# Kernel optimization log

Hardware: AMD Instinct MI355X
Metric: run time of the kernel (lower is better)

The kernel has to match this reference:

```python
import jax, jax.numpy as jnp
import numpy as np

N, E, D, H, G, L = 50000, 800000, 64, 2, 512, 3  # nodes, edges, hidden, heads, graphs, layers


def setup_inputs() -> dict:
    key = jax.random.key(0)
    ks = jax.random.split(key, 20)
    x = jax.random.normal(ks[0], (N, D), dtype=jnp.float32)
    edge_index = jax.random.randint(ks[1], (2, E), 0, N, dtype=jnp.int64)
    batch = jnp.sort(jax.random.randint(ks[2], (N,), 0, G, dtype=jnp.int64))
    s = 1.0 / np.sqrt(D)
    Wq = jax.random.normal(ks[3], (L, D, H * D), dtype=jnp.float32) * s
    bq = jnp.zeros((L, H * D), jnp.float32)
    Wk = jax.random.normal(ks[4], (L, D, H * D), dtype=jnp.float32) * s
    bk = jnp.zeros((L, H * D), jnp.float32)
    Wv = jax.random.normal(ks[5], (L, D, H * D), dtype=jnp.float32) * s
    bv = jnp.zeros((L, H * D), jnp.float32)
    Ws = jax.random.normal(ks[6], (L, D, D), dtype=jnp.float32) * s
    bs = jnp.zeros((L, D), jnp.float32)
    ln_g = jnp.ones((L - 1, D), jnp.float32)
    ln_b = jnp.zeros((L - 1, D), jnp.float32)
    Wout = jax.random.normal(ks[7], (D, 1), dtype=jnp.float32) * s
    bout = jnp.zeros((1,), jnp.float32)
    return {"x": x, "edge_index": edge_index, "batch": batch, "num_graphs": G,
            "Wq": Wq, "bq": bq, "Wk": Wk, "bk": bk, "Wv": Wv, "bv": bv,
            "Ws": Ws, "bs": bs, "ln_g": ln_g, "ln_b": ln_b, "Wout": Wout, "bout": bout}


def _transformer_conv(x, src, dst, Wq, bq, Wk, bk, Wv, bv, Ws, bs):
    n = x.shape[0]
    q = (x @ Wq + bq).reshape(n, H, D)
    k = (x @ Wk + bk).reshape(n, H, D)
    v = (x @ Wv + bv).reshape(n, H, D)
    # per-edge attention score: q_dst . k_src / sqrt(d)
    scores = jnp.einsum('ehc,ehc->eh', q[dst], k[src]) / jnp.sqrt(jnp.float32(D))
    m = jax.ops.segment_max(scores, dst, num_segments=n)          # [n,H]
    e = jnp.exp(scores - m[dst])
    denom = jax.ops.segment_sum(e, dst, num_segments=n)           # [n,H]
    alpha = e / (denom[dst] + 1e-16)
    msg = alpha[..., None] * v[src]                               # [E,H,D]
    out = jax.ops.segment_sum(msg, dst, num_segments=n)           # [n,H,D]
    return out.mean(axis=1) + x @ Ws + bs                         # concat=False: head mean + skip


def _layernorm(x, g, b):
    mu = x.mean(-1, keepdims=True)
    var = ((x - mu) ** 2).mean(-1, keepdims=True)
    return (x - mu) / jnp.sqrt(var + 1e-5) * g + b


def reference(x, edge_index, batch, num_graphs, Wq, bq, Wk, bk, Wv, bv, Ws, bs, ln_g, ln_b, Wout, bout):
    src, dst = edge_index[0], edge_index[1]
    h = x
    for i in range(L):
        h = _transformer_conv(h, src, dst, Wq[i], bq[i], Wk[i], bk[i], Wv[i], bv[i], Ws[i], bs[i])
        h = jax.nn.relu(h)
        if i != L - 1:
            h = _layernorm(h, ln_g[i], ln_b[i])
    # global mean pool over graphs
    sums = jax.ops.segment_sum(h, batch, num_segments=num_graphs)
    cnt = jax.ops.segment_sum(jnp.ones((h.shape[0],), h.dtype), batch, num_segments=num_graphs)
    pooled = sums / jnp.maximum(cnt, 1.0)[:, None]
    return pooled @ Wout + bout
```

## Files before the change

kernel.cpp:

```cpp
#include <hip/hip_runtime.h>
#include <hip/hip_fp16.h>
#include <math.h>

#define NN 50000
#define EE 800000
#define GG 512

typedef _Float16 f16x8 __attribute__((ext_vector_type(8)));
typedef float f32x4 __attribute__((ext_vector_type(4)));

__device__ __forceinline__ float wave16_sum(float p) {
    p += __shfl_xor(p, 1);
    p += __shfl_xor(p, 2);
    p += __shfl_xor(p, 4);
    p += __shfl_xor(p, 8);
    return p;
}
__device__ __forceinline__ float dot4(float4 a, float4 b) {
    return a.x * b.x + a.y * b.y + a.z * b.z + a.w * b.w;
}
__device__ __forceinline__ float2 h2f(unsigned int u) {
    __half2 h = *reinterpret_cast<__half2*>(&u);
    return __half22float2(h);
}
__device__ __forceinline__ unsigned short f2us(float x) {
    return __half_as_ushort(__float2half(x));
}
__device__ __forceinline__ float us2f(unsigned short u) {
    return __half2float(__ushort_as_half(u));
}

__global__ void deg_kernel(const int* __restrict__ ei, int* __restrict__ deg) {
    int e = blockIdx.x * 256 + threadIdx.x;
    if (e < EE) atomicAdd(&deg[ei[EE + e]], 1);
}

__global__ void scan1(const int* __restrict__ deg, int* __restrict__ incl, int* __restrict__ bsum) {
    __shared__ int sh[256];
    int t = threadIdx.x;
    int n = blockIdx.x * 256 + t;
    int vv = (n < NN) ? deg[n] : 0;
    sh[t] = vv; __syncthreads();
    for (int off = 1; off < 256; off <<= 1) {
        int u = (t >= off) ? sh[t - off] : 0;
        __syncthreads();
        sh[t] += u;
        __syncthreads();
    }
    if (n < NN) incl[n] = sh[t];
    if (t == 255) bsum[blockIdx.x] = sh[255];
}

__global__ void scan2(int* __restrict__ bsum, int nblk) {
    __shared__ int sh[256];
    int t = threadIdx.x;
    int vv = (t < nblk) ? bsum[t] : 0;
    sh[t] = vv; __syncthreads();
    for (int off = 1; off < 256; off <<= 1) {
        int u = (t >= off) ? sh[t - off] : 0;
        __syncthreads();
        sh[t] += u;
        __syncthreads();
    }
    bsum[t] = sh[t];
}

__global__ void scan3(int* __restrict__ rowst, const int* __restrict__ deg,
                      const int* __restrict__ bsum, int* __restrict__ cursor) {
    int n = blockIdx.x * 256 + threadIdx.x;
    if (n >= NN) return;
    int off = (blockIdx.x > 0) ? bsum[blockIdx.x - 1] : 0;
    int excl = rowst[n] - deg[n] + off;
    rowst[n] = excl;
    cursor[n] = excl;
}

__global__ void fill_kernel(const int* __restrict__ ei, int* __restrict__ cursor,
                            int* __restrict__ esrc) {
    int e = blockIdx.x * 256 + threadIdx.x;
    if (e < EE) {
        int s = ei[e], d = ei[EE + e];
        int pos = atomicAdd(&cursor[d], 1);
        esrc[pos] = s;
    }
}

__global__ void cast_x_kernel(const float* __restrict__ x, unsigned short* __restrict__ xh) {
    int i = blockIdx.x * 256 + threadIdx.x;
    if (i < NN * 16) {
        float4 v = *(const float4*)(x + (size_t)i * 4);
        ushort4 o = make_ushort4(f2us(v.x), f2us(v.y), f2us(v.z), f2us(v.w));
        *(ushort4*)(xh + (size_t)i * 4) = o;
    }
}

#define WT_LSTRIDE (448 * 64)
__global__ void pack_w_kernel(const float* __restrict__ Wq, const float* __restrict__ Wk,
                              const float* __restrict__ Wv, const float* __restrict__ Ws,
                              unsigned short* __restrict__ wt) {
    int idx = blockIdx.x * 256 + threadIdx.x;
    if (idx >= 3 * WT_LSTRIDE) return;
    int l = idx / WT_LSTRIDE, r = idx % WT_LSTRIDE;
    int c = r / 64, k = r % 64;
    float val;
    if (c < 384) {
        int m = c >> 7, col = c & 127;
        const float* W = (m == 0) ? Wq : ((m == 1) ? Wk : Wv);
        val = W[(size_t)l * 64 * 128 + k * 128 + col];
    } else {
        int col = c - 384;
        val = Ws[(size_t)l * 64 * 64 + k * 64 + col];
    }
    wt[idx] = f2us(val);
}

__global__ __launch_bounds__(256) void gemm_mfma(
    const unsigned short* __restrict__ xh,
    const unsigned short* __restrict__ wt,
    const float* __restrict__ bq, const float* __restrict__ bk,
    const float* __restrict__ bv, const float* __restrict__ bsk,
    float* __restrict__ q, unsigned short* __restrict__ kvh,
    float* __restrict__ skip) {
    int t = threadIdx.x;
    int wave = t >> 6, lane = t & 63;
    int li = lane & 15, lh = lane >> 4;
    int row0 = blockIdx.x * 32 + (wave & 1) * 16;
    int ctbase = (wave >> 1) * 14;

    int arow = min(row0 + li, NN - 1);
    const unsigned short* ap = xh + (size_t)arow * 64 + lh * 8;
    f16x8 a0 = *(const f16x8*)(ap);
    f16x8 a1 = *(const f16x8*)(ap + 32);

    int rb = row0 + lh * 4;

    #pragma unroll 2
    for (int tt = 0; tt < 14; ++tt) {
        int c = (ctbase + tt) * 16 + li;
        const unsigned short* bp = wt + (size_t)c * 64 + lh * 8;
        f16x8 b0 = *(const f16x8*)(bp);
        f16x8 b1 = *(const f16x8*)(bp + 32);
        f32x4 d = {0.f, 0.f, 0.f, 0.f};
        d = __builtin_amdgcn_mfma_f32_16x16x32_f16(a0, b0, d, 0, 0, 0);
        d = __builtin_amdgcn_mfma_f32_16x16x32_f16(a1, b1, d, 0, 0, 0);
        if (c < 128) {
            float bias = bq[c];
            #pragma unroll
            for (int e = 0; e < 4; ++e) {
                int r = rb + e;
                if (r < NN) q[(size_t)r * 128 + c] = d[e] + bias;
            }
        } else if (c < 256) {
            int ch = c - 128;
            float bias = bk[ch];
            int off = (ch < 64) ? ((ch >> 2) * 16 + (ch & 3))
                                : (((ch - 64) >> 2) * 16 + 4 + (ch & 3));
            #pragma unroll
            for (int e = 0; e < 4; ++e) {
                int r = rb + e;
                if (r < NN) kvh[(size_t)r * 256 + off] = f2us(d[e] + bias);
            }
        } else if (c < 384) {
            int ch = c - 256;
            float bias = bv[ch];
            int off = 8 + ((ch < 64) ? ((ch >> 2) * 16 + (ch & 3))
                                     : (((ch - 64) >> 2) * 16 + 4 + (ch & 3)));
            #pragma unroll
            for (int e = 0; e < 4; ++e) {
                int r = rb + e;
                if (r < NN) kvh[(size_t)r * 256 + off] = f2us(d[e] + bias);
            }
        } else {
            int ch = c - 384;
            float bias = bsk[ch];
            #pragma unroll
            for (int e = 0; e < 4; ++e) {
                int r = rb + e;
                if (r < NN) skip[(size_t)r * 64 + ch] = d[e] + bias;
            }
        }
    }
}

__global__ __launch_bounds__(256) void agg_kernel(
    const float* __restrict__ q, const unsigned short* __restrict__ kvh,
    const float* __restrict__ skip,
    const int* __restrict__ rowst, const int* __restrict__ deg,
    const int* __restrict__ esrc, const float* __restrict__ gamma,
    const float* __restrict__ beta, unsigned short* __restrict__ hout, int do_ln) {
    int wave = threadIdx.x >> 6;
    int lane = threadIdx.x & 63;
    int node = blockIdx.x * 4 + wave;
    if (node >= NN) return;
    int j = lane & 15;
    int slot = lane >> 4;

    float4 q0 = *(const float4*)(q + (size_t)node * 128 + j * 4);
    float4 q1 = *(const float4*)(q + (size_t)node * 128 + 64 + j * 4);
    float m0 = -1e30f, m1 = -1e30f;
    float l0 = 0.f, l1 = 0.f;
    float acc0[4] = {0.f, 0.f, 0.f, 0.f};
    float acc1[4] = {0.f, 0.f, 0.f, 0.f};

    int st = rowst[node];
    int dg = deg[node];
    for (int base = slot * 2; base < dg; base += 8) {
        int last = dg - 1;
        int s0 = esrc[st + min(base + 0, last)];
        int s1 = esrc[st + min(base + 1, last)];
        const unsigned short* b0 = kvh + (size_t)s0 * 256 + j * 16;
        const unsigned short* b1 = kvh + (size_t)s1 * 256 + j * 16;
        uint4 A0 = *(const uint4*)(b0);
        uint4 B0 = *(const uint4*)(b0 + 8);
        uint4 A1 = *(const uint4*)(b1);
        uint4 B1 = *(const uint4*)(b1 + 8);

        float2 a00 = h2f(A0.x), a01 = h2f(A0.y), a02 = h2f(A0.z), a03 = h2f(A0.w);
        float2 a10 = h2f(A1.x), a11 = h2f(A1.y), a12 = h2f(A1.z), a13 = h2f(A1.w);
        float4 k00 = {a00.x, a00.y, a01.x, a01.y};
        float4 k01 = {a02.x, a02.y, a03.x, a03.y};
        float4 k10 = {a10.x, a10.y, a11.x, a11.y};
        float4 k11 = {a12.x, a12.y, a13.x, a13.y};

        float p00 = wave16_sum(dot4(q0, k00)) * 0.125f;
        float p01 = wave16_sum(dot4(q1, k01)) * 0.125f;
        float p10 = wave16_sum(dot4(q0, k10)) * 0.125f;
        float p11 = wave16_sum(dot4(q1, k11)) * 0.125f;
        if (base + 1 > last) { p10 = -1e30f; p11 = -1e30f; }

        float2 c00 = h2f(B0.x), c01 = h2f(B0.y), c02 = h2f(B0.z), c03 = h2f(B0.w);
        float2 c10 = h2f(B1.x), c11 = h2f(B1.y), c12 = h2f(B1.z), c13 = h2f(B1.w);
        float v00[4] = {c00.x, c00.y, c01.x, c01.y};
        float v01[4] = {c02.x, c02.y, c03.x, c03.y};
        float v10[4] = {c10.x, c10.y, c11.x, c11.y};
        float v11[4] = {c12.x, c12.y, c13.x, c13.y};

        {
            float nm = fmaxf(m0, fmaxf(p00, p10));
            float f = __expf(m0 - nm);
            float e0 = __expf(p00 - nm);
            float e1 = __expf(p10 - nm);
            l0 = l0 * f + e0 + e1;
            #pragma unroll
            for (int r = 0; r < 4; ++r)
                acc0[r] = acc0[r] * f + e0 * v00[r] + e1 * v10[r];
            m0 = nm;
        }
        {
            float nm = fmaxf(m1, fmaxf(p01, p11));
            float f = __expf(m1 - nm);
            float e0 = __expf(p01 - nm);
            float e1 = __expf(p11 - nm);
            l1 = l1 * f + e0 + e1;
            #pragma unroll
            for (int r = 0; r < 4; ++r)
                acc1[r] = acc1[r] * f + e0 * v01[r] + e1 * v11[r];
            m1 = nm;
        }
    }
    #pragma unroll
    for (int mask = 16; mask <= 32; mask <<= 1) {
        {
            float mo = __shfl_xor(m0, mask);
            float lo = __shfl_xor(l0, mask);
            float ao[4];
            #pragma unroll
            for (int r = 0; r < 4; ++r) ao[r] = __shfl_xor(acc0[r], mask);
            float nm = fmaxf(m0, mo);
            float fa = __expf(m0 - nm);
            float fb = __expf(mo - nm);
            l0 = l0 * fa + lo * fb;
            #pragma unroll
            for (int r = 0; r < 4; ++r) acc0[r] = acc0[r] * fa + ao[r] * fb;
            m0 = nm;
        }
        {
            float mo = __shfl_xor(m1, mask);
            float lo = __shfl_xor(l1, mask);
            float ao[4];
            #pragma unroll
            for (int r = 0; r < 4; ++r) ao[r] = __shfl_xor(acc1[r], mask);
            float nm = fmaxf(m1, mo);
            float fa = __expf(m1 - nm);
            float fb = __expf(mo - nm);
            l1 = l1 * fa + lo * fb;
            #pragma unroll
            for (int r = 0; r < 4; ++r) acc1[r] = acc1[r] * fa + ao[r] * fb;
            m1 = nm;
        }
    }
    float i0 = 1.f / (l0 + 1e-16f);
    float i1 = 1.f / (l1 + 1e-16f);
    float4 sk = *(const float4*)(skip + (size_t)node * 64 + j * 4);
    float ska[4] = {sk.x, sk.y, sk.z, sk.w};
    float val[4];
    #pragma unroll
    for (int r = 0; r < 4; ++r) {
        float o = 0.5f * (acc0[r] * i0 + acc1[r] * i1) + ska[r];
        val[r] = fmaxf(o, 0.f);
    }
    if (do_ln) {
        float s = val[0] + val[1] + val[2] + val[3];
        s = wave16_sum(s);
        float mu = s * (1.f / 64.f);
        float ss = 0.f;
        #pragma unroll
        for (int r = 0; r < 4; ++r) { float d = val[r] - mu; ss += d * d; }
        ss = wave16_sum(ss);
        float rstd = rsqrtf(ss * (1.f / 64.f) + 1e-5f);
        float4 g4 = *(const float4*)(gamma + j * 4);
        float4 b4 = *(const float4*)(beta + j * 4);
        float ga[4] = {g4.x, g4.y, g4.z, g4.w};
        float ba[4] = {b4.x, b4.y, b4.z, b4.w};
        #pragma unroll
        for (int r = 0; r < 4; ++r) val[r] = (val[r] - mu) * rstd * ga[r] + ba[r];
    }
    if (slot == 0) {
        ushort4 o = make_ushort4(f2us(val[0]), f2us(val[1]), f2us(val[2]), f2us(val[3]));
        *(ushort4*)(hout + (size_t)node * 64 + j * 4) = o;
    }
}

__device__ __forceinline__ int lbound(const int* __restrict__ a, int n, int key) {
    int lo = 0, hi = n;
    while (lo < hi) {
        int mid = (lo + hi) >> 1;
        if (a[mid] < key) lo = mid + 1; else hi = mid;
    }
    return lo;
}

__global__ __launch_bounds__(256) void pool_final_kernel(
    const unsigned short* __restrict__ h, const int* __restrict__ batch,
    const float* __restrict__ Wout, const float* __restrict__ bout,
    float* __restrict__ out) {
    __shared__ int sh_lo, sh_hi;
    __shared__ float part[4][64];
    int g = blockIdx.x;
    int t = threadIdx.x;
    if (t == 0) {
        sh_lo = lbound(batch, NN, g);
        sh_hi = lbound(batch, NN, g + 1);
    }
    __syncthreads();
    int lo = sh_lo, hi = sh_hi;
    int c = t & 63, w = t >> 6;
    float s = 0.f;
    for (int n = lo + w; n < hi; n += 4) s += us2f(h[(size_t)n * 64 + c]);
    part[w][c] = s;
    __syncthreads();
    if (t < 64) {
        float tot = part[0][t] + part[1][t] + part[2][t] + part[3][t];
        float cnt = (float)(hi - lo);
        float val = tot / fmaxf(cnt, 1.f) * Wout[t];
        #pragma unroll
        for (int mk = 1; mk < 64; mk <<= 1) val += __shfl_xor(val, mk);
        if (t == 0) out[g] = val + bout[0];
    }
}

extern "C" void kernel_launch(void* const* d_in, const int* in_sizes, int n_in,
                              void* d_out, int out_size, void* d_ws, size_t ws_size,
                              hipStream_t stream) {
    const float* x    = (const float*)d_in[0];
    const int*   ei   = (const int*)d_in[1];
    const int*   batch= (const int*)d_in[2];
    const float* Wq   = (const float*)d_in[4];
    const float* bq   = (const float*)d_in[5];
    const float* Wk   = (const float*)d_in[6];
    const float* bk   = (const float*)d_in[7];
    const float* Wv   = (const float*)d_in[8];
    const float* bv   = (const float*)d_in[9];
    const float* Ws   = (const float*)d_in[10];
    const float* bs   = (const float*)d_in[11];
    const float* lng  = (const float*)d_in[12];
    const float* lnb  = (const float*)d_in[13];
    const float* Wout = (const float*)d_in[14];
    const float* bout = (const float*)d_in[15];
    float* out = (float*)d_out;

    float* q    = (float*)d_ws;
    unsigned short* kvh = (unsigned short*)(q + (size_t)NN * 128);
    float* skip = (float*)(kvh + (size_t)NN * 256);
    unsigned short* xh0 = (unsigned short*)(skip + (size_t)NN * 64);
    unsigned short* xh1 = xh0 + (size_t)NN * 64;
    unsigned short* wt  = xh1 + (size_t)NN * 64;
    int* deg    = (int*)(wt + 3 * WT_LSTRIDE);
    int* rowst  = deg + NN;
    int* cursor = rowst + NN;
    int* bsum   = cursor + NN;
    int* esrc   = bsum + 256;

    hipMemsetAsync(deg, 0, NN * sizeof(int), stream);

    const int NB = (NN + 255) / 256;
    deg_kernel<<<(EE + 255) / 256, 256, 0, stream>>>(ei, deg);
    scan1<<<NB, 256, 0, stream>>>(deg, rowst, bsum);
    scan2<<<1, 256, 0, stream>>>(bsum, NB);
    scan3<<<NB, 256, 0, stream>>>(rowst, deg, bsum, cursor);
    fill_kernel<<<(EE + 255) / 256, 256, 0, stream>>>(ei, cursor, esrc);

    cast_x_kernel<<<(NN * 16 + 255) / 256, 256, 0, stream>>>(x, xh0);
    pack_w_kernel<<<(3 * WT_LSTRIDE + 255) / 256, 256, 0, stream>>>(Wq, Wk, Wv, Ws, wt);

    const int GEMM_GRID = (NN + 31) / 32;
    unsigned short* hin = xh0;
    unsigned short* houts[3] = {xh1, xh0, xh1};
    for (int l = 0; l < 3; ++l) {
        gemm_mfma<<<GEMM_GRID, 256, 0, stream>>>(hin, wt + (size_t)l * WT_LSTRIDE,
            bq + (size_t)l * 128, bk + (size_t)l * 128, bv + (size_t)l * 128,
            bs + (size_t)l * 64, q, kvh, skip);
        int do_ln = (l < 2) ? 1 : 0;
        agg_kernel<<<(NN + 3) / 4, 256, 0, stream>>>(q, kvh, skip, rowst, deg, esrc,
                                                     lng + (size_t)(do_ln ? l : 0) * 64,
                                                     lnb + (size_t)(do_ln ? l : 0) * 64,
                                                     houts[l], do_ln);
        hin = houts[l];
    }
    pool_final_kernel<<<GG, 256, 0, stream>>>(hin, batch, Wout, bout, out);
}
```

Measured before the change: 417.9 us.

## Store Q in fp16 with prescaled log2e factor, use fdot2 and exp2, 16-bit edge indices

Q is stored in half precision, premultiplied by 1/sqrt(D)*log2(e), so attention scores can use exp2 directly and fp16 dot2 instructions. Source indices in the CSR are stored as 16-bit values. Together these cut memory traffic for the Q and edge-index reads and reduce ALU work in the aggregation loop. The cost is lower precision in the scores, and the 16-bit indices only hold for node counts below 65536.

```diff
diff --git a/kernel.cpp b/kernel.cpp
--- a/kernel.cpp
+++ b/kernel.cpp
@@ -7,7 +7,16 @@
 #define GG 512
 
 typedef _Float16 f16x8 __attribute__((ext_vector_type(8)));
+typedef _Float16 f16x2 __attribute__((ext_vector_type(2)));
 typedef float f32x4 __attribute__((ext_vector_type(4)));
+
+#if defined(__has_builtin)
+#if __has_builtin(__builtin_amdgcn_fdot2)
+#define HAS_FDOT2 1
+#endif
+#endif
+
+#define QSCALE 0.1803368801111244f
 
 __device__ __forceinline__ float wave16_sum(float p) {
     p += __shfl_xor(p, 1);
@@ -16,9 +25,6 @@
     p += __shfl_xor(p, 8);
     return p;
 }
-__device__ __forceinline__ float dot4(float4 a, float4 b) {
-    return a.x * b.x + a.y * b.y + a.z * b.z + a.w * b.w;
-}
 __device__ __forceinline__ float2 h2f(unsigned int u) {
     __half2 h = *reinterpret_cast<__half2*>(&u);
     return __half22float2(h);
@@ -28,6 +34,19 @@
 }
 __device__ __forceinline__ float us2f(unsigned short u) {
     return __half2float(__ushort_as_half(u));
+}
+__device__ __forceinline__ f16x2 u2h2(unsigned int u) {
+    union { unsigned int u; f16x2 h; } x; x.u = u; return x.h;
+}
+__device__ __forceinline__ float dot2acc(f16x2 a, f16x2 b, float c) {
+#ifdef HAS_FDOT2
+    return __builtin_amdgcn_fdot2(a, b, c, false);
+#else
+    return c + (float)a[0] * (float)b[0] + (float)a[1] * (float)b[1];
+#endif
+}
+__device__ __forceinline__ float exp2fast(float x) {
+    return __builtin_amdgcn_exp2f(x);
 }
 
 __global__ void deg_kernel(const int* __restrict__ ei, int* __restrict__ deg) {
@@ -76,12 +95,12 @@
 }
 
 __global__ void fill_kernel(const int* __restrict__ ei, int* __restrict__ cursor,
-                            int* __restrict__ esrc) {
+                            unsigned short* __restrict__ esrc) {
     int e = blockIdx.x * 256 + threadIdx.x;
     if (e < EE) {
         int s = ei[e], d = ei[EE + e];
         int pos = atomicAdd(&cursor[d], 1);
-        esrc[pos] = s;
+        esrc[pos] = (unsigned short)s;
     }
 }
 
@@ -119,7 +138,7 @@
     const unsigned short* __restrict__ wt,
     const float* __restrict__ bq, const float* __restrict__ bk,
     const float* __restrict__ bv, const float* __restrict__ bsk,
-    float* __restrict__ q, unsigned short* __restrict__ kvh,
+    unsigned short* __restrict__ qh, unsigned short* __restrict__ kvh,
     float* __restrict__ skip) {
     int t = threadIdx.x;
     int wave = t >> 6, lane = t & 63;
@@ -148,7 +167,7 @@
             #pragma unroll
             for (int e = 0; e < 4; ++e) {
                 int r = rb + e;
-                if (r < NN) q[(size_t)r * 128 + c] = d[e] + bias;
+                if (r < NN) qh[(size_t)r * 128 + c] = f2us((d[e] + bias) * QSCALE);
             }
         } else if (c < 256) {
             int ch = c - 128;
@@ -183,10 +202,10 @@
 }
 
 __global__ __launch_bounds__(256) void agg_kernel(
-    const float* __restrict__ q, const unsigned short* __restrict__ kvh,
+    const unsigned short* __restrict__ qh, const unsigned short* __restrict__ kvh,
     const float* __restrict__ skip,
     const int* __restrict__ rowst, const int* __restrict__ deg,
-    const int* __restrict__ esrc, const float* __restrict__ gamma,
+    const unsigned short* __restrict__ esrc, const float* __restrict__ gamma,
     const float* __restrict__ beta, unsigned short* __restrict__ hout, int do_ln) {
     int wave = threadIdx.x >> 6;
     int lane = threadIdx.x & 63;
@@ -195,8 +214,11 @@
     int j = lane & 15;
     int slot = lane >> 4;
 
-    float4 q0 = *(const float4*)(q + (size_t)node * 128 + j * 4);
-    float4 q1 = *(const float4*)(q + (size_t)node * 128 + 64 + j * 4);
+    uint2 qu0 = *(const uint2*)(qh + (size_t)node * 128 + j * 4);
+    uint2 qu1 = *(const uint2*)(qh + (size_t)node * 128 + 64 + j * 4);
+    f16x2 q0a = u2h2(qu0.x), q0b = u2h2(qu0.y);
+    f16x2 q1a = u2h2(qu1.x), q1b = u2h2(qu1.y);
+
     float m0 = -1e30f, m1 = -1e30f;
     float l0 = 0.f, l1 = 0.f;
     float acc0[4] = {0.f, 0.f, 0.f, 0.f};
@@ -206,8 +228,8 @@
     int dg = deg[node];
     for (int base = slot * 2; base < dg; base += 8) {
         int last = dg - 1;
-        int s0 = esrc[st + min(base + 0, last)];
-        int s1 = esrc[st + min(base + 1, last)];
+        int s0 = (int)esrc[st + min(base + 0, last)];
+        int s1 = (int)esrc[st + min(base + 1, last)];
         const unsigned short* b0 = kvh + (size_t)s0 * 256 + j * 16;
         const unsigned short* b1 = kvh + (size_t)s1 * 256 + j * 16;
         uint4 A0 = *(const uint4*)(b0);
@@ -215,17 +237,14 @@
         uint4 A1 = *(const uint4*)(b1);
         uint4 B1 = *(const uint4*)(b1 + 8);
 
-        float2 a00 = h2f(A0.x), a01 = h2f(A0.y), a02 = h2f(A0.z), a03 = h2f(A0.w);
-        float2 a10 = h2f(A1.x), a11 = h2f(A1.y), a12 = h2f(A1.z), a13 = h2f(A1.w);
-        float4 k00 = {a00.x, a00.y, a01.x, a01.y};
-        float4 k01 = {a02.x, a02.y, a03.x, a03.y};
-        float4 k10 = {a10.x, a10.y, a11.x, a11.y};
-        float4 k11 = {a12.x, a12.y, a13.x, a13.y};
-
-        float p00 = wave16_sum(dot4(q0, k00)) * 0.125f;
-        float p01 = wave16_sum(dot4(q1, k01)) * 0.125f;
-        float p10 = wave16_sum(dot4(q0, k10)) * 0.125f;
-        float p11 = wave16_sum(dot4(q1, k11)) * 0.125f;
+        float p00 = dot2acc(q0b, u2h2(A0.y), dot2acc(q0a, u2h2(A0.x), 0.f));
+        float p01 = dot2acc(q1b, u2h2(A0.w), dot2acc(q1a, u2h2(A0.z), 0.f));
+        float p10 = dot2acc(q0b, u2h2(A1.y), dot2acc(q0a, u2h2(A1.x), 0.f));
+        float p11 = dot2acc(q1b, u2h2(A1.w), dot2acc(q1a, u2h2(A1.z), 0.f));
+        p00 = wave16_sum(p00);
+        p01 = wave16_sum(p01);
+        p10 = wave16_sum(p10);
+        p11 = wave16_sum(p11);
         if (base + 1 > last) { p10 = -1e30f; p11 = -1e30f; }
 
         float2 c00 = h2f(B0.x), c01 = h2f(B0.y), c02 = h2f(B0.z), c03 = h2f(B0.w);
@@ -237,9 +256,9 @@
 
         {
             float nm = fmaxf(m0, fmaxf(p00, p10));
-            float f = __expf(m0 - nm);
-            float e0 = __expf(p00 - nm);
-            float e1 = __expf(p10 - nm);
+            float f = exp2fast(m0 - nm);
+            float e0 = exp2fast(p00 - nm);
+            float e1 = exp2fast(p10 - nm);
             l0 = l0 * f + e0 + e1;
             #pragma unroll
             for (int r = 0; r < 4; ++r)
@@ -248,9 +267,9 @@
         }
         {
             float nm = fmaxf(m1, fmaxf(p01, p11));
-            float f = __expf(m1 - nm);
-            float e0 = __expf(p01 - nm);
-            float e1 = __expf(p11 - nm);
+            float f = exp2fast(m1 - nm);
+            float e0 = exp2fast(p01 - nm);
+            float e1 = exp2fast(p11 - nm);
             l1 = l1 * f + e0 + e1;
             #pragma unroll
             for (int r = 0; r < 4; ++r)
@@ -267,8 +286,8 @@
             #pragma unroll
             for (int r = 0; r < 4; ++r) ao[r] = __shfl_xor(acc0[r], mask);
             float nm = fmaxf(m0, mo);
-            float fa = __expf(m0 - nm);
-            float fb = __expf(mo - nm);
+            float fa = exp2fast(m0 - nm);
+            float fb = exp2fast(mo - nm);
             l0 = l0 * fa + lo * fb;
             #pragma unroll
             for (int r = 0; r < 4; ++r) acc0[r] = acc0[r] * fa + ao[r] * fb;
@@ -281,8 +300,8 @@
             #pragma unroll
             for (int r = 0; r < 4; ++r) ao[r] = __shfl_xor(acc1[r], mask);
             float nm = fmaxf(m1, mo);
-            float fa = __expf(m1 - nm);
-            float fb = __expf(mo - nm);
+            float fa = exp2fast(m1 - nm);
+            float fb = exp2fast(mo - nm);
             l1 = l1 * fa + lo * fb;
             #pragma unroll
             for (int r = 0; r < 4; ++r) acc1[r] = acc1[r] * fa + ao[r] * fb;
@@ -379,8 +398,8 @@
     const float* bout = (const float*)d_in[15];
     float* out = (float*)d_out;
 
-    float* q    = (float*)d_ws;
-    unsigned short* kvh = (unsigned short*)(q + (size_t)NN * 128);
+    unsigned short* qh  = (unsigned short*)d_ws;
+    unsigned short* kvh = qh + (size_t)NN * 128;
     float* skip = (float*)(kvh + (size_t)NN * 256);
     unsigned short* xh0 = (unsigned short*)(skip + (size_t)NN * 64);
     unsigned short* xh1 = xh0 + (size_t)NN * 64;
@@ -389,7 +408,7 @@
     int* rowst  = deg + NN;
     int* cursor = rowst + NN;
     int* bsum   = cursor + NN;
-    int* esrc   = bsum + 256;
+    unsigned short* esrc = (unsigned short*)(bsum + 256);
 
     hipMemsetAsync(deg, 0, NN * sizeof(int), stream);
 
@@ -409,9 +428,9 @@
     for (int l = 0; l < 3; ++l) {
         gemm_mfma<<<GEMM_GRID, 256, 0, stream>>>(hin, wt + (size_t)l * WT_LSTRIDE,
             bq + (size_t)l * 128, bk + (size_t)l * 128, bv + (size_t)l * 128,
-            bs + (size_t)l * 64, q, kvh, skip);
+            bs + (size_t)l * 64, qh, kvh, skip);
         int do_ln = (l < 2) ? 1 : 0;
-        agg_kernel<<<(NN + 3) / 4, 256, 0, stream>>>(q, kvh, skip, rowst, deg, esrc,
+        agg_kernel<<<(NN + 3) / 4, 256, 0, stream>>>(qh, kvh, skip, rowst, deg, esrc,
                                                      lng + (size_t)(do_ln ? l : 0) * 64,
                                                      lnb + (size_t)(do_ln ? l : 0) * 64,
                                                      houts[l], do_ln);
```

Result: faster. 404.7 us (-3.2%).
